# Optimization experiments

Measured on AMD Instinct MI355X. Metric: run time of the kernel, lower is better.

The kernel has to match this reference:

```python
import jax, jax.numpy as jnp
import numpy as np
from jax import lax


def _log_g(z):
    # log of g(x) = x + 0.5 if x >= 0 else sigmoid(x)
    return jnp.where(z >= 0, jnp.log(jax.nn.relu(z) + 0.5), -jax.nn.softplus(-z))


def setup_inputs() -> dict:
    key = jax.random.key(0)
    k1, k2, k3 = jax.random.split(key, 3)
    B, S, D, H = 8, 8192, 512, 256
    x = jax.random.normal(k1, (B, S, D), dtype=jnp.float32)
    h_prev = jax.random.normal(k2, (B, H), dtype=jnp.float32)
    # nn.Linear(D, 3H, bias=False) weight: [3H, D], scaled like torch default init
    W = jax.random.normal(k3, (3 * H, D), dtype=jnp.float32) * (1.0 / np.sqrt(D))
    return {"x": x, "h_prev": h_prev, "W": W}


def reference(x, h_prev, W):
    # x: [B,S,D], h_prev: [B,H], W: [3H,D]
    seq_len = x.shape[1]
    y = jnp.einsum("bsd,hd->bsh", x, W)              # [B,S,3H]
    f, i, h = jnp.split(y, 3, axis=-1)                # each [B,S,H]
    diff = jax.nn.softplus(-f) - jax.nn.softplus(-i)
    log_f = -jax.nn.softplus(diff)                    # log(sigmoid-normalized forget gate)
    log_i = -jax.nn.softplus(-diff)                   # log(input gate)
    log_h0 = _log_g(h_prev)                           # [B,H]
    log_tilde_h = _log_g(h)                           # [B,S,H]
    # parallel scan in log space: h_t = f_t * h_{t-1} + i_t * g(h_t~)
    a_star = jnp.concatenate(
        [jnp.zeros_like(log_h0)[:, None], jnp.cumsum(log_f, axis=1)], axis=1
    )                                                  # [B,S+1,H]
    log_vals = jnp.concatenate([log_h0[:, None], log_i + log_tilde_h], axis=1)  # [B,S+1,H]
    log_h = a_star + lax.cumlogsumexp(log_vals - a_star, axis=1)
    h_t = jnp.exp(log_h)                               # [B,S+1,H]
    return h_t[:, -seq_len:]                           # [B,S,H]
```

## Files before the change

### kernel.cpp

```cpp
#include <hip/hip_runtime.h>
#include <math.h>

#define BB 8
#define SS 8192
#define DD 512
#define HH 256
#define MM (BB * SS)
#define NN 768
#define CC 64
#define LL 128

typedef unsigned short u16;
typedef __attribute__((ext_vector_type(8))) short short8;
typedef __attribute__((ext_vector_type(4))) float f32x4;

#define AS1(p) ((const __attribute__((address_space(1))) void*)(p))
#define AS3(p) ((__attribute__((address_space(3))) void*)(p))

__device__ __forceinline__ u16 f2bf_rtne(float f) {
    union { float f; unsigned u; } v; v.f = f;
    unsigned r = v.u + 0x7fffu + ((v.u >> 16) & 1u);
    return (u16)(r >> 16);
}
__device__ __forceinline__ unsigned pack2_rtn(float a, float b) {
    union { float f; unsigned u; } x, y; x.f = a; y.f = b;
    return ((x.u + 0x8000u) >> 16) | ((y.u + 0x8000u) & 0xffff0000u);
}

__device__ __forceinline__ float sp_fast(float z) {
    return (z > 15.0f) ? z : __logf(1.0f + __expf(z));
}

__global__ __launch_bounds__(256) void convert_W(const float* __restrict__ W,
                                                 u16* __restrict__ Wr) {
    const int chunk = blockIdx.x * 256 + threadIdx.x;
    const int kh = chunk / 1536;
    const int rem = chunk % 1536;
    const int cl = rem >> 2, qq = rem & 3;
    const int kc = kh >> 1, half = kh & 1;
    const int c = half * 384 + cl;
    const int hg = c / 48, r48 = c % 48;
    const int g = r48 >> 4, hl = r48 & 15;
    const int wrow = g * HH + hg * 16 + hl;
    const int k0 = kc * 32 + qq * 8;
    const float4 v0 = *(const float4*)&W[(size_t)wrow * DD + k0];
    const float4 v1 = *(const float4*)&W[(size_t)wrow * DD + k0 + 4];
    u16 o[8];
    o[0]=f2bf_rtne(v0.x); o[1]=f2bf_rtne(v0.y); o[2]=f2bf_rtne(v0.z); o[3]=f2bf_rtne(v0.w);
    o[4]=f2bf_rtne(v1.x); o[5]=f2bf_rtne(v1.y); o[6]=f2bf_rtne(v1.z); o[7]=f2bf_rtne(v1.w);
    *(uint4*)&Wr[(size_t)chunk * 8] = *(const uint4*)o;
}

__global__ __launch_bounds__(512) void gemm_gate_mfma(
    const float* __restrict__ x,
    const u16* __restrict__ Wr,
    float* __restrict__ F_arr,
    float* __restrict__ u_out)
{
    __shared__ __align__(16) u16 Bs[2][12288];
    __shared__ __align__(16) u16 As[2][64 * 40];

    const int tid = threadIdx.x;
    const int m0 = blockIdx.x * 64;
    const int w = tid >> 6;
    const int lane = tid & 63;
    const int l16 = lane & 15;
    const int quad = lane >> 4;

    const int arow = tid >> 3;
    const int aqi = tid & 7;

    f32x4 acc[4][6];
    #pragma unroll
    for (int a = 0; a < 4; ++a)
        #pragma unroll
        for (int b = 0; b < 6; ++b)
            #pragma unroll
            for (int e = 0; e < 4; ++e) acc[a][b][e] = 0.0f;

    #pragma unroll
    for (int i = 0; i < 3; ++i) {
        const int idx = i * 512 + tid;
        __builtin_amdgcn_global_load_lds(AS1(Wr + (size_t)idx * 8),
                                         AS3(&Bs[0][idx * 8]), 16, 0, 0);
    }
    {
        const float4 v = *(const float4*)&x[(size_t)(m0 + arow) * DD + aqi * 4];
        *(uint2*)&As[0][arow * 40 + aqi * 4] =
            make_uint2(pack2_rtn(v.x, v.y), pack2_rtn(v.z, v.w));
    }
    float4 a_reg = *(const float4*)&x[(size_t)(m0 + arow) * DD + 32 + aqi * 4];
    __syncthreads();

    for (int kc = 0; kc < 16; ++kc) {
        {
            const size_t base = ((size_t)(kc * 2 + 1)) * 12288;
            #pragma unroll
            for (int i = 0; i < 3; ++i) {
                const int idx = i * 512 + tid;
                __builtin_amdgcn_global_load_lds(AS1(Wr + base + (size_t)idx * 8),
                                                 AS3(&Bs[1][idx * 8]), 16, 0, 0);
            }
        }
        short8 afr[4];
        #pragma unroll
        for (int mf = 0; mf < 4; ++mf)
            afr[mf] = *(const short8*)&As[kc & 1][(mf * 16 + l16) * 40 + quad * 8];

        {
            short8 bfr[3];
            #pragma unroll
            for (int jn = 0; jn < 3; ++jn)
                bfr[jn] = *(const short8*)&Bs[0][((w * 3 + jn) * 16 + l16) * 32 + quad * 8];
            #pragma unroll
            for (int mf = 0; mf < 4; ++mf)
                #pragma unroll
                for (int jn = 0; jn < 3; ++jn)
                    acc[mf][jn] = __builtin_amdgcn_mfma_f32_16x16x32_bf16(
                        afr[mf], bfr[jn], acc[mf][jn], 0, 0, 0);
        }
        *(uint2*)&As[(kc + 1) & 1][arow * 40 + aqi * 4] =
            make_uint2(pack2_rtn(a_reg.x, a_reg.y), pack2_rtn(a_reg.z, a_reg.w));
        {
            const int knext = (kc + 2 < 16) ? (kc + 2) : 15;
            a_reg = *(const float4*)&x[(size_t)(m0 + arow) * DD + knext * 32 + aqi * 4];
        }
        __syncthreads();

        if (kc < 15) {
            const size_t base = ((size_t)((kc + 1) * 2)) * 12288;
            #pragma unroll
            for (int i = 0; i < 3; ++i) {
                const int idx = i * 512 + tid;
                __builtin_amdgcn_global_load_lds(AS1(Wr + base + (size_t)idx * 8),
                                                 AS3(&Bs[0][idx * 8]), 16, 0, 0);
            }
        }
        {
            short8 bfr[3];
            #pragma unroll
            for (int jn = 0; jn < 3; ++jn)
                bfr[jn] = *(const short8*)&Bs[1][((w * 3 + jn) * 16 + l16) * 32 + quad * 8];
            #pragma unroll
            for (int mf = 0; mf < 4; ++mf)
                #pragma unroll
                for (int jn = 0; jn < 3; ++jn)
                    acc[mf][3 + jn] = __builtin_amdgcn_mfma_f32_16x16x32_bf16(
                        afr[mf], bfr[jn], acc[mf][3 + jn], 0, 0, 0);
        }
        __syncthreads();
    }

    #pragma unroll
    for (int half = 0; half < 2; ++half) {
        const int head = (half * 8 + w) * 16 + l16;
        #pragma unroll
        for (int mf = 0; mf < 4; ++mf) {
            #pragma unroll
            for (int r = 0; r < 4; ++r) {
                const int m = m0 + mf * 16 + quad * 4 + r;
                const float fr = acc[mf][half * 3 + 0][r];
                const float ir = acc[mf][half * 3 + 1][r];
                const float hr = acc[mf][half * 3 + 2][r];
                const float diff = sp_fast(-fr) - sp_fast(-ir);
                const float F = __builtin_amdgcn_rcpf(1.0f + __expf(diff));
                const float I = 1.0f - F;
                const float G = (hr >= 0.0f) ? (hr + 0.5f)
                                             : __builtin_amdgcn_rcpf(1.0f + __expf(-hr));
                const size_t o = (size_t)m * HH + head;
                F_arr[o] = F;
                u_out[o] = I * G;
            }
        }
    }
}

__global__ __launch_bounds__(256) void scan_pass1(
    const float* __restrict__ F_arr, const float* __restrict__ u_arr,
    float* __restrict__ P_arr, float* __restrict__ U_arr) {
    const int bc = blockIdx.x;
    const int b = bc / CC;
    const int c = bc % CC;
    const int h = threadIdx.x;
    size_t base = ((size_t)(b * SS + c * LL)) * HH + h;
    float P = 1.0f, U = 0.0f;
    #pragma unroll 4
    for (int t = 0; t < LL; ++t) {
        const float F = F_arr[base];
        const float u = u_arr[base];
        U = F * U + u;
        P = P * F;
        base += HH;
    }
    const size_t o = ((size_t)c * BB + b) * HH + h;
    P_arr[o] = P;
    U_arr[o] = U;
}

__global__ __launch_bounds__(256) void scan_pass2(
    const float* __restrict__ h_prev, const float* __restrict__ P_arr,
    const float* __restrict__ U_arr, float* __restrict__ Hin) {
    const int b = blockIdx.x;
    const int h = threadIdx.x;
    const float z = h_prev[b * HH + h];
    float carry = (z >= 0.0f) ? (z + 0.5f) : __builtin_amdgcn_rcpf(1.0f + __expf(-z));
    for (int c = 0; c < CC; ++c) {
        const size_t o = ((size_t)c * BB + b) * HH + h;
        Hin[o] = carry;
        carry = P_arr[o] * carry + U_arr[o];
    }
}

__global__ __launch_bounds__(256) void scan_pass3(
    const float* __restrict__ F_arr, const float* __restrict__ Hin,
    float* __restrict__ out) {
    const int bc = blockIdx.x;
    const int b = bc / CC;
    const int c = bc % CC;
    const int h = threadIdx.x;
    float hv = Hin[((size_t)c * BB + b) * HH + h];
    size_t base = ((size_t)(b * SS + c * LL)) * HH + h;
    #pragma unroll 4
    for (int t = 0; t < LL; ++t) {
        const float F = F_arr[base];
        const float u = out[base];
        hv = F * hv + u;
        out[base] = hv;
        base += HH;
    }
}

extern "C" void kernel_launch(void* const* d_in, const int* in_sizes, int n_in,
                              void* d_out, int out_size, void* d_ws, size_t ws_size,
                              hipStream_t stream) {
    const float* x      = (const float*)d_in[0];
    const float* h_prev = (const float*)d_in[1];
    const float* W      = (const float*)d_in[2];

    float* F_arr = (float*)d_ws;
    float* P_arr = F_arr + (size_t)MM * HH;
    float* U_arr = P_arr + (size_t)CC * BB * HH;
    float* Hin   = U_arr + (size_t)CC * BB * HH;
    u16*   Wr    = (u16*)(Hin + (size_t)CC * BB * HH);

    convert_W<<<192, 256, 0, stream>>>(W, Wr);
    gemm_gate_mfma<<<MM / 64, 512, 0, stream>>>(x, Wr, F_arr, (float*)d_out);
    scan_pass1<<<BB * CC, HH, 0, stream>>>(F_arr, (const float*)d_out, P_arr, U_arr);
    scan_pass2<<<BB, HH, 0, stream>>>(h_prev, P_arr, U_arr, Hin);
    scan_pass3<<<BB * CC, HH, 0, stream>>>(F_arr, Hin, (float*)d_out);
}
```

Baseline: 350.9 us.

## Triple-buffer GEMM W tiles with swizzled LDS and vectorize scan passes

The GEMM moves from double to triple buffering of the bf16 weight tiles in LDS. It uses explicit waitcnt/s_barrier pairs with sched barriers and raised MFMA priority, so global-to-LDS loads run further ahead of compute. The weight layout is XOR-swizzled in both convert_W and the fragment reads to reduce LDS bank conflicts. Separately, the scan passes now have each thread handle two adjacent hidden units with float2 loads and stores, using half as many blocks, and pass2 gets an unroll pragma. The hand-written vmcnt counts are fragile and a wrong count could let a tile be read before it has landed.

```diff
diff --git a/kernel.cpp b/kernel.cpp
--- a/kernel.cpp
+++ b/kernel.cpp
@@ -35,8 +35,9 @@
                                                  u16* __restrict__ Wr) {
     const int chunk = blockIdx.x * 256 + threadIdx.x;
     const int kh = chunk / 1536;
-    const int rem = chunk % 1536;
-    const int cl = rem >> 2, qq = rem & 3;
+    const int u = chunk % 1536;
+    const int cl = ((u >> 2) & ~1) | (((u >> 2) ^ (u >> 4)) & 1);
+    const int qq = (u & 3) ^ (cl & 3);
     const int kc = kh >> 1, half = kh & 1;
     const int c = half * 384 + cl;
     const int hg = c / 48, r48 = c % 48;
@@ -57,7 +58,7 @@
     float* __restrict__ F_arr,
     float* __restrict__ u_out)
 {
-    __shared__ __align__(16) u16 Bs[2][12288];
+    __shared__ __align__(16) u16 Bs[3][12288];
     __shared__ __align__(16) u16 As[2][64 * 40];
 
     const int tid = threadIdx.x;
@@ -78,77 +79,144 @@
             #pragma unroll
             for (int e = 0; e < 4; ++e) acc[a][b][e] = 0.0f;
 
+    int boff[3];
+    #pragma unroll
+    for (int jn = 0; jn < 3; ++jn) {
+        const int r = (w * 3 + jn) * 16 + l16;
+        boff[jn] = ((r * 4 + quad) ^ (r & 7)) * 8;
+    }
+
+    const float* xrow = &x[(size_t)(m0 + arow) * DD];
+
+    const float4 v0 = *(const float4*)&xrow[aqi * 4];
+    float4 a_reg = *(const float4*)&xrow[32 + aqi * 4];
+    asm volatile("" ::: "memory");
     #pragma unroll
     for (int i = 0; i < 3; ++i) {
         const int idx = i * 512 + tid;
         __builtin_amdgcn_global_load_lds(AS1(Wr + (size_t)idx * 8),
                                          AS3(&Bs[0][idx * 8]), 16, 0, 0);
     }
-    {
-        const float4 v = *(const float4*)&x[(size_t)(m0 + arow) * DD + aqi * 4];
-        *(uint2*)&As[0][arow * 40 + aqi * 4] =
-            make_uint2(pack2_rtn(v.x, v.y), pack2_rtn(v.z, v.w));
-    }
-    float4 a_reg = *(const float4*)&x[(size_t)(m0 + arow) * DD + 32 + aqi * 4];
-    __syncthreads();
-
-    for (int kc = 0; kc < 16; ++kc) {
-        {
-            const size_t base = ((size_t)(kc * 2 + 1)) * 12288;
-            #pragma unroll
-            for (int i = 0; i < 3; ++i) {
-                const int idx = i * 512 + tid;
-                __builtin_amdgcn_global_load_lds(AS1(Wr + base + (size_t)idx * 8),
-                                                 AS3(&Bs[1][idx * 8]), 16, 0, 0);
-            }
-        }
-        short8 afr[4];
+    #pragma unroll
+    for (int i = 0; i < 3; ++i) {
+        const int idx = i * 512 + tid;
+        __builtin_amdgcn_global_load_lds(AS1(Wr + 12288 + (size_t)idx * 8),
+                                         AS3(&Bs[1][idx * 8]), 16, 0, 0);
+    }
+    *(uint2*)&As[0][arow * 40 + aqi * 4] =
+        make_uint2(pack2_rtn(v0.x, v0.y), pack2_rtn(v0.z, v0.w));
+
+    int cur = 0;
+    short8 afr[4];
+    for (int kc = 0; kc < 15; ++kc) {
+        const int nb1 = (cur + 2 > 2) ? cur - 1 : cur + 2;
+        const int c1  = (cur + 1 > 2) ? 0 : cur + 1;
+
+        asm volatile("s_waitcnt lgkmcnt(0)" ::: "memory");
+        asm volatile("s_waitcnt vmcnt(3)" ::: "memory");
+        __builtin_amdgcn_s_barrier();
+        __builtin_amdgcn_sched_barrier(0);
         #pragma unroll
         for (int mf = 0; mf < 4; ++mf)
             afr[mf] = *(const short8*)&As[kc & 1][(mf * 16 + l16) * 40 + quad * 8];
-
-        {
-            short8 bfr[3];
-            #pragma unroll
-            for (int jn = 0; jn < 3; ++jn)
-                bfr[jn] = *(const short8*)&Bs[0][((w * 3 + jn) * 16 + l16) * 32 + quad * 8];
-            #pragma unroll
-            for (int mf = 0; mf < 4; ++mf)
-                #pragma unroll
-                for (int jn = 0; jn < 3; ++jn)
-                    acc[mf][jn] = __builtin_amdgcn_mfma_f32_16x16x32_bf16(
-                        afr[mf], bfr[jn], acc[mf][jn], 0, 0, 0);
-        }
+        short8 bfr[3];
+        #pragma unroll
+        for (int jn = 0; jn < 3; ++jn)
+            bfr[jn] = *(const short8*)&Bs[cur][boff[jn]];
         *(uint2*)&As[(kc + 1) & 1][arow * 40 + aqi * 4] =
             make_uint2(pack2_rtn(a_reg.x, a_reg.y), pack2_rtn(a_reg.z, a_reg.w));
         {
             const int knext = (kc + 2 < 16) ? (kc + 2) : 15;
-            a_reg = *(const float4*)&x[(size_t)(m0 + arow) * DD + knext * 32 + aqi * 4];
+            a_reg = *(const float4*)&xrow[knext * 32 + aqi * 4];
         }
-        __syncthreads();
-
-        if (kc < 15) {
-            const size_t base = ((size_t)((kc + 1) * 2)) * 12288;
+        {
+            const size_t gbase = (size_t)(2 * kc + 2) * 12288;
             #pragma unroll
             for (int i = 0; i < 3; ++i) {
                 const int idx = i * 512 + tid;
-                __builtin_amdgcn_global_load_lds(AS1(Wr + base + (size_t)idx * 8),
-                                                 AS3(&Bs[0][idx * 8]), 16, 0, 0);
+                __builtin_amdgcn_global_load_lds(AS1(Wr + gbase + (size_t)idx * 8),
+                                                 AS3(&Bs[nb1][idx * 8]), 16, 0, 0);
             }
         }
+        __builtin_amdgcn_sched_barrier(0);
+        __builtin_amdgcn_s_setprio(1);
+        #pragma unroll
+        for (int mf = 0; mf < 4; ++mf)
+            #pragma unroll
+            for (int jn = 0; jn < 3; ++jn)
+                acc[mf][jn] = __builtin_amdgcn_mfma_f32_16x16x32_bf16(
+                    afr[mf], bfr[jn], acc[mf][jn], 0, 0, 0);
+        __builtin_amdgcn_s_setprio(0);
+
+        asm volatile("s_waitcnt lgkmcnt(0)" ::: "memory");
+        asm volatile("s_waitcnt vmcnt(4)" ::: "memory");
+        __builtin_amdgcn_s_barrier();
+        __builtin_amdgcn_sched_barrier(0);
+        #pragma unroll
+        for (int jn = 0; jn < 3; ++jn)
+            bfr[jn] = *(const short8*)&Bs[c1][boff[jn]];
         {
-            short8 bfr[3];
+            const size_t gbase = (size_t)(2 * kc + 3) * 12288;
+            #pragma unroll
+            for (int i = 0; i < 3; ++i) {
+                const int idx = i * 512 + tid;
+                __builtin_amdgcn_global_load_lds(AS1(Wr + gbase + (size_t)idx * 8),
+                                                 AS3(&Bs[cur][idx * 8]), 16, 0, 0);
+            }
+        }
+        __builtin_amdgcn_sched_barrier(0);
+        __builtin_amdgcn_s_setprio(1);
+        #pragma unroll
+        for (int mf = 0; mf < 4; ++mf)
             #pragma unroll
             for (int jn = 0; jn < 3; ++jn)
-                bfr[jn] = *(const short8*)&Bs[1][((w * 3 + jn) * 16 + l16) * 32 + quad * 8];
-            #pragma unroll
-            for (int mf = 0; mf < 4; ++mf)
-                #pragma unroll
-                for (int jn = 0; jn < 3; ++jn)
-                    acc[mf][3 + jn] = __builtin_amdgcn_mfma_f32_16x16x32_bf16(
-                        afr[mf], bfr[jn], acc[mf][3 + jn], 0, 0, 0);
-        }
-        __syncthreads();
+                acc[mf][3 + jn] = __builtin_amdgcn_mfma_f32_16x16x32_bf16(
+                    afr[mf], bfr[jn], acc[mf][3 + jn], 0, 0, 0);
+        __builtin_amdgcn_s_setprio(0);
+
+        cur = nb1;
+    }
+    asm volatile("" :: "v"(a_reg.x), "v"(a_reg.y), "v"(a_reg.z), "v"(a_reg.w));
+
+    asm volatile("s_waitcnt lgkmcnt(0)" ::: "memory");
+    asm volatile("s_waitcnt vmcnt(3)" ::: "memory");
+    __builtin_amdgcn_s_barrier();
+    __builtin_amdgcn_sched_barrier(0);
+    #pragma unroll
+    for (int mf = 0; mf < 4; ++mf)
+        afr[mf] = *(const short8*)&As[1][(mf * 16 + l16) * 40 + quad * 8];
+    {
+        short8 bfr[3];
+        #pragma unroll
+        for (int jn = 0; jn < 3; ++jn)
+            bfr[jn] = *(const short8*)&Bs[cur][boff[jn]];
+        __builtin_amdgcn_s_setprio(1);
+        #pragma unroll
+        for (int mf = 0; mf < 4; ++mf)
+            #pragma unroll
+            for (int jn = 0; jn < 3; ++jn)
+                acc[mf][jn] = __builtin_amdgcn_mfma_f32_16x16x32_bf16(
+                    afr[mf], bfr[jn], acc[mf][jn], 0, 0, 0);
+        __builtin_amdgcn_s_setprio(0);
+    }
+    asm volatile("s_waitcnt lgkmcnt(0)" ::: "memory");
+    asm volatile("s_waitcnt vmcnt(0)" ::: "memory");
+    __builtin_amdgcn_s_barrier();
+    __builtin_amdgcn_sched_barrier(0);
+    {
+        const int c1 = (cur + 1 > 2) ? 0 : cur + 1;
+        short8 bfr[3];
+        #pragma unroll
+        for (int jn = 0; jn < 3; ++jn)
+            bfr[jn] = *(const short8*)&Bs[c1][boff[jn]];
+        __builtin_amdgcn_s_setprio(1);
+        #pragma unroll
+        for (int mf = 0; mf < 4; ++mf)
+            #pragma unroll
+            for (int jn = 0; jn < 3; ++jn)
+                acc[mf][3 + jn] = __builtin_amdgcn_mfma_f32_16x16x32_bf16(
+                    afr[mf], bfr[jn], acc[mf][3 + jn], 0, 0, 0);
+        __builtin_amdgcn_s_setprio(0);
     }
 
     #pragma unroll
@@ -178,23 +246,25 @@
 __global__ __launch_bounds__(256) void scan_pass1(
     const float* __restrict__ F_arr, const float* __restrict__ u_arr,
     float* __restrict__ P_arr, float* __restrict__ U_arr) {
-    const int bc = blockIdx.x;
-    const int b = bc / CC;
-    const int c = bc % CC;
-    const int h = threadIdx.x;
-    size_t base = ((size_t)(b * SS + c * LL)) * HH + h;
-    float P = 1.0f, U = 0.0f;
-    #pragma unroll 4
+    const int pair = blockIdx.x * 2 + (threadIdx.x >> 7);
+    const int b = pair / CC;
+    const int c = pair % CC;
+    const int h0 = (threadIdx.x & 127) * 2;
+    size_t base = ((size_t)(b * SS + c * LL)) * HH + h0;
+    float P0 = 1.0f, P1 = 1.0f, U0 = 0.0f, U1 = 0.0f;
+    #pragma unroll 8
     for (int t = 0; t < LL; ++t) {
-        const float F = F_arr[base];
-        const float u = u_arr[base];
-        U = F * U + u;
-        P = P * F;
+        const float2 F = *(const float2*)&F_arr[base];
+        const float2 u = *(const float2*)&u_arr[base];
+        U0 = F.x * U0 + u.x;
+        U1 = F.y * U1 + u.y;
+        P0 *= F.x;
+        P1 *= F.y;
         base += HH;
     }
-    const size_t o = ((size_t)c * BB + b) * HH + h;
-    P_arr[o] = P;
-    U_arr[o] = U;
+    const size_t o = ((size_t)c * BB + b) * HH + h0;
+    *(float2*)&P_arr[o] = make_float2(P0, P1);
+    *(float2*)&U_arr[o] = make_float2(U0, U1);
 }
 
 __global__ __launch_bounds__(256) void scan_pass2(
@@ -204,6 +274,7 @@
     const int h = threadIdx.x;
     const float z = h_prev[b * HH + h];
     float carry = (z >= 0.0f) ? (z + 0.5f) : __builtin_amdgcn_rcpf(1.0f + __expf(-z));
+    #pragma unroll 4
     for (int c = 0; c < CC; ++c) {
         const size_t o = ((size_t)c * BB + b) * HH + h;
         Hin[o] = carry;
@@ -214,18 +285,19 @@
 __global__ __launch_bounds__(256) void scan_pass3(
     const float* __restrict__ F_arr, const float* __restrict__ Hin,
     float* __restrict__ out) {
-    const int bc = blockIdx.x;
-    const int b = bc / CC;
-    const int c = bc % CC;
-    const int h = threadIdx.x;
-    float hv = Hin[((size_t)c * BB + b) * HH + h];
-    size_t base = ((size_t)(b * SS + c * LL)) * HH + h;
-    #pragma unroll 4
+    const int pair = blockIdx.x * 2 + (threadIdx.x >> 7);
+    const int b = pair / CC;
+    const int c = pair % CC;
+    const int h0 = (threadIdx.x & 127) * 2;
+    float2 hv = *(const float2*)&Hin[((size_t)c * BB + b) * HH + h0];
+    size_t base = ((size_t)(b * SS + c * LL)) * HH + h0;
+    #pragma unroll 8
     for (int t = 0; t < LL; ++t) {
-        const float F = F_arr[base];
-        const float u = out[base];
-        hv = F * hv + u;
-        out[base] = hv;
+        const float2 F = *(const float2*)&F_arr[base];
+        const float2 u = *(const float2*)&out[base];
+        hv.x = F.x * hv.x + u.x;
+        hv.y = F.y * hv.y + u.y;
+        *(float2*)&out[base] = hv;
         base += HH;
     }
 }
@@ -245,7 +317,7 @@
 
     convert_W<<<192, 256, 0, stream>>>(W, Wr);
     gemm_gate_mfma<<<MM / 64, 512, 0, stream>>>(x, Wr, F_arr, (float*)d_out);
-    scan_pass1<<<BB * CC, HH, 0, stream>>>(F_arr, (const float*)d_out, P_arr, U_arr);
+    scan_pass1<<<BB * CC / 2, 256, 0, stream>>>(F_arr, (const float*)d_out, P_arr, U_arr);
     scan_pass2<<<BB, HH, 0, stream>>>(h_prev, P_arr, U_arr, Hin);
-    scan_pass3<<<BB * CC, HH, 0, stream>>>(F_arr, Hin, (float*)d_out);
-}
+    scan_pass3<<<BB * CC / 2, 256, 0, stream>>>(F_arr, Hin, (float*)d_out);
+}
```

Measured after the change: 339.1 us. -3.4%, faster.

## Pack F/u as half2 in output buffer, split GEMM N across blocks, shorter scan chunks

Applied to the files above, without the earlier changes.

The gate GEMM now writes F and u as a packed fp16 pair into the output buffer instead of two fp32 arrays. This halves the intermediate traffic and drops the separate F workspace. The GEMM is split into four column blocks with 256 threads, an XOR-swizzled W layout, block-index remapping and s_setprio around the MFMAs. The scan uses 256 chunks of 32 steps and processes two heads per thread with vector loads. The fp16 storage of F and u lowers precision, which may hurt accuracy over long products, and the serial pass2 now runs four times more iterations.

```diff
diff --git a/kernel.cpp b/kernel.cpp
--- a/kernel.cpp
+++ b/kernel.cpp
@@ -1,4 +1,5 @@
 #include <hip/hip_runtime.h>
+#include <hip/hip_fp16.h>
 #include <math.h>
 
 #define BB 8
@@ -7,8 +8,8 @@
 #define HH 256
 #define MM (BB * SS)
 #define NN 768
-#define CC 64
-#define LL 128
+#define CC 256
+#define LL 32
 
 typedef unsigned short u16;
 typedef __attribute__((ext_vector_type(8))) short short8;
@@ -31,18 +32,30 @@
     return (z > 15.0f) ? z : __logf(1.0f + __expf(z));
 }
 
+__device__ __forceinline__ unsigned packFu(float F, float u) {
+    __half2 h = __floats2half2_rn(F, u);
+    return *reinterpret_cast<unsigned*>(&h);
+}
+__device__ __forceinline__ float2 unpackFu(unsigned v) {
+    __half2 h = *reinterpret_cast<__half2*>(&v);
+    return __half22float2(h);
+}
+
 __global__ __launch_bounds__(256) void convert_W(const float* __restrict__ W,
                                                  u16* __restrict__ Wr) {
     const int chunk = blockIdx.x * 256 + threadIdx.x;
-    const int kh = chunk / 1536;
-    const int rem = chunk % 1536;
-    const int cl = rem >> 2, qq = rem & 3;
-    const int kc = kh >> 1, half = kh & 1;
-    const int c = half * 384 + cl;
-    const int hg = c / 48, r48 = c % 48;
-    const int g = r48 >> 4, hl = r48 & 15;
-    const int wrow = g * HH + hg * 16 + hl;
-    const int k0 = kc * 32 + qq * 8;
+    const int kcb = chunk / 768;
+    const int u = chunk % 768;
+    const int kc = kcb >> 2, cb = kcb & 3;
+    const int v = u & 31;
+    const int s = ((v >> 2) & 7) ^ ((v >> 4) & 1);
+    const int q = (v & 3) ^ (s & 3);
+    const int r = ((u >> 5) << 3) | s;
+    const int w = r / 48;
+    const int rr = r % 48;
+    const int jn = rr >> 4, hl = rr & 15;
+    const int wrow = jn * HH + cb * 64 + w * 16 + hl;
+    const int k0 = kc * 32 + q * 8;
     const float4 v0 = *(const float4*)&W[(size_t)wrow * DD + k0];
     const float4 v1 = *(const float4*)&W[(size_t)wrow * DD + k0 + 4];
     u16 o[8];
@@ -51,150 +64,144 @@
     *(uint4*)&Wr[(size_t)chunk * 8] = *(const uint4*)o;
 }
 
-__global__ __launch_bounds__(512) void gemm_gate_mfma(
+__global__ __launch_bounds__(256, 4) void gemm_gate_mfma(
     const float* __restrict__ x,
     const u16* __restrict__ Wr,
-    float* __restrict__ F_arr,
-    float* __restrict__ u_out)
+    unsigned* __restrict__ Fu)
 {
-    __shared__ __align__(16) u16 Bs[2][12288];
+    __shared__ __align__(16) u16 Bs[2][6144];
     __shared__ __align__(16) u16 As[2][64 * 40];
 
     const int tid = threadIdx.x;
-    const int m0 = blockIdx.x * 64;
+    const int L = (blockIdx.x & 7) * 512 + (blockIdx.x >> 3);
+    const int mblk = L >> 2, cb = L & 3;
+    const int m0 = mblk * 64;
+
     const int w = tid >> 6;
     const int lane = tid & 63;
     const int l16 = lane & 15;
     const int quad = lane >> 4;
 
-    const int arow = tid >> 3;
-    const int aqi = tid & 7;
-
-    f32x4 acc[4][6];
+    const int arow = tid >> 2;
+    const int aqi = tid & 3;
+
+    f32x4 acc[4][3];
     #pragma unroll
     for (int a = 0; a < 4; ++a)
         #pragma unroll
-        for (int b = 0; b < 6; ++b)
+        for (int b = 0; b < 3; ++b)
             #pragma unroll
             for (int e = 0; e < 4; ++e) acc[a][b][e] = 0.0f;
 
+    int boff[3];
     #pragma unroll
-    for (int i = 0; i < 3; ++i) {
-        const int idx = i * 512 + tid;
-        __builtin_amdgcn_global_load_lds(AS1(Wr + (size_t)idx * 8),
-                                         AS3(&Bs[0][idx * 8]), 16, 0, 0);
-    }
+    for (int jn = 0; jn < 3; ++jn) {
+        const int r = w * 48 + jn * 16 + l16;
+        boff[jn] = (((r * 4 + quad) ^ (r & 7))) * 8;
+    }
+
+    const float* xrow = &x[(size_t)(m0 + arow) * DD];
+
     {
-        const float4 v = *(const float4*)&x[(size_t)(m0 + arow) * DD + aqi * 4];
-        *(uint2*)&As[0][arow * 40 + aqi * 4] =
-            make_uint2(pack2_rtn(v.x, v.y), pack2_rtn(v.z, v.w));
-    }
-    float4 a_reg = *(const float4*)&x[(size_t)(m0 + arow) * DD + 32 + aqi * 4];
+        const size_t ub = (size_t)(0 * 4 + cb) * 768;
+        #pragma unroll
+        for (int i = 0; i < 3; ++i) {
+            const int idx = i * 256 + tid;
+            __builtin_amdgcn_global_load_lds(AS1(Wr + (ub + idx) * 8),
+                                             AS3(&Bs[0][idx * 8]), 16, 0, 0);
+        }
+    }
+    float4 va0 = *(const float4*)&xrow[aqi * 8];
+    float4 va1 = *(const float4*)&xrow[aqi * 8 + 4];
+    float4 ar0 = *(const float4*)&xrow[32 + aqi * 8];
+    float4 ar1 = *(const float4*)&xrow[32 + aqi * 8 + 4];
+    {
+        uint4 p;
+        p.x = pack2_rtn(va0.x, va0.y); p.y = pack2_rtn(va0.z, va0.w);
+        p.z = pack2_rtn(va1.x, va1.y); p.w = pack2_rtn(va1.z, va1.w);
+        *(uint4*)&As[0][arow * 40 + aqi * 8] = p;
+    }
     __syncthreads();
 
     for (int kc = 0; kc < 16; ++kc) {
-        {
-            const size_t base = ((size_t)(kc * 2 + 1)) * 12288;
+        const int buf = kc & 1;
+        if (kc < 15) {
+            const size_t ub = (size_t)((kc + 1) * 4 + cb) * 768;
             #pragma unroll
             for (int i = 0; i < 3; ++i) {
-                const int idx = i * 512 + tid;
-                __builtin_amdgcn_global_load_lds(AS1(Wr + base + (size_t)idx * 8),
-                                                 AS3(&Bs[1][idx * 8]), 16, 0, 0);
+                const int idx = i * 256 + tid;
+                __builtin_amdgcn_global_load_lds(AS1(Wr + (ub + idx) * 8),
+                                                 AS3(&Bs[buf ^ 1][idx * 8]), 16, 0, 0);
+            }
+            uint4 p;
+            p.x = pack2_rtn(ar0.x, ar0.y); p.y = pack2_rtn(ar0.z, ar0.w);
+            p.z = pack2_rtn(ar1.x, ar1.y); p.w = pack2_rtn(ar1.z, ar1.w);
+            *(uint4*)&As[buf ^ 1][arow * 40 + aqi * 8] = p;
+            if (kc < 14) {
+                ar0 = *(const float4*)&xrow[(kc + 2) * 32 + aqi * 8];
+                ar1 = *(const float4*)&xrow[(kc + 2) * 32 + aqi * 8 + 4];
             }
         }
         short8 afr[4];
         #pragma unroll
         for (int mf = 0; mf < 4; ++mf)
-            afr[mf] = *(const short8*)&As[kc & 1][(mf * 16 + l16) * 40 + quad * 8];
-
-        {
-            short8 bfr[3];
+            afr[mf] = *(const short8*)&As[buf][(mf * 16 + l16) * 40 + quad * 8];
+        short8 bfr[3];
+        #pragma unroll
+        for (int jn = 0; jn < 3; ++jn)
+            bfr[jn] = *(const short8*)&Bs[buf][boff[jn]];
+
+        __builtin_amdgcn_s_setprio(1);
+        #pragma unroll
+        for (int mf = 0; mf < 4; ++mf)
             #pragma unroll
             for (int jn = 0; jn < 3; ++jn)
-                bfr[jn] = *(const short8*)&Bs[0][((w * 3 + jn) * 16 + l16) * 32 + quad * 8];
-            #pragma unroll
-            for (int mf = 0; mf < 4; ++mf)
-                #pragma unroll
-                for (int jn = 0; jn < 3; ++jn)
-                    acc[mf][jn] = __builtin_amdgcn_mfma_f32_16x16x32_bf16(
-                        afr[mf], bfr[jn], acc[mf][jn], 0, 0, 0);
+                acc[mf][jn] = __builtin_amdgcn_mfma_f32_16x16x32_bf16(
+                    afr[mf], bfr[jn], acc[mf][jn], 0, 0, 0);
+        __builtin_amdgcn_s_setprio(0);
+        __syncthreads();
+    }
+
+    const int head = cb * 64 + w * 16 + l16;
+    #pragma unroll
+    for (int mf = 0; mf < 4; ++mf) {
+        #pragma unroll
+        for (int r = 0; r < 4; ++r) {
+            const int m = m0 + mf * 16 + quad * 4 + r;
+            const float fr = acc[mf][0][r];
+            const float ir = acc[mf][1][r];
+            const float hr = acc[mf][2][r];
+            const float diff = sp_fast(-fr) - sp_fast(-ir);
+            const float F = __builtin_amdgcn_rcpf(1.0f + __expf(diff));
+            const float I = 1.0f - F;
+            const float G = (hr >= 0.0f) ? (hr + 0.5f)
+                                         : __builtin_amdgcn_rcpf(1.0f + __expf(-hr));
+            Fu[(size_t)m * HH + head] = packFu(F, I * G);
         }
-        *(uint2*)&As[(kc + 1) & 1][arow * 40 + aqi * 4] =
-            make_uint2(pack2_rtn(a_reg.x, a_reg.y), pack2_rtn(a_reg.z, a_reg.w));
-        {
-            const int knext = (kc + 2 < 16) ? (kc + 2) : 15;
-            a_reg = *(const float4*)&x[(size_t)(m0 + arow) * DD + knext * 32 + aqi * 4];
-        }
-        __syncthreads();
-
-        if (kc < 15) {
-            const size_t base = ((size_t)((kc + 1) * 2)) * 12288;
-            #pragma unroll
-            for (int i = 0; i < 3; ++i) {
-                const int idx = i * 512 + tid;
-                __builtin_amdgcn_global_load_lds(AS1(Wr + base + (size_t)idx * 8),
-                                                 AS3(&Bs[0][idx * 8]), 16, 0, 0);
-            }
-        }
-        {
-            short8 bfr[3];
-            #pragma unroll
-            for (int jn = 0; jn < 3; ++jn)
-                bfr[jn] = *(const short8*)&Bs[1][((w * 3 + jn) * 16 + l16) * 32 + quad * 8];
-            #pragma unroll
-            for (int mf = 0; mf < 4; ++mf)
-                #pragma unroll
-                for (int jn = 0; jn < 3; ++jn)
-                    acc[mf][3 + jn] = __builtin_amdgcn_mfma_f32_16x16x32_bf16(
-                        afr[mf], bfr[jn], acc[mf][3 + jn], 0, 0, 0);
-        }
-        __syncthreads();
-    }
-
-    #pragma unroll
-    for (int half = 0; half < 2; ++half) {
-        const int head = (half * 8 + w) * 16 + l16;
-        #pragma unroll
-        for (int mf = 0; mf < 4; ++mf) {
-            #pragma unroll
-            for (int r = 0; r < 4; ++r) {
-                const int m = m0 + mf * 16 + quad * 4 + r;
-                const float fr = acc[mf][half * 3 + 0][r];
-                const float ir = acc[mf][half * 3 + 1][r];
-                const float hr = acc[mf][half * 3 + 2][r];
-                const float diff = sp_fast(-fr) - sp_fast(-ir);
-                const float F = __builtin_amdgcn_rcpf(1.0f + __expf(diff));
-                const float I = 1.0f - F;
-                const float G = (hr >= 0.0f) ? (hr + 0.5f)
-                                             : __builtin_amdgcn_rcpf(1.0f + __expf(-hr));
-                const size_t o = (size_t)m * HH + head;
-                F_arr[o] = F;
-                u_out[o] = I * G;
-            }
-        }
     }
 }
 
 __global__ __launch_bounds__(256) void scan_pass1(
-    const float* __restrict__ F_arr, const float* __restrict__ u_arr,
+    const unsigned* __restrict__ Fu,
     float* __restrict__ P_arr, float* __restrict__ U_arr) {
-    const int bc = blockIdx.x;
-    const int b = bc / CC;
-    const int c = bc % CC;
-    const int h = threadIdx.x;
-    size_t base = ((size_t)(b * SS + c * LL)) * HH + h;
-    float P = 1.0f, U = 0.0f;
-    #pragma unroll 4
+    const int pair = blockIdx.x * 2 + (threadIdx.x >> 7);
+    const int b = pair / CC;
+    const int c = pair % CC;
+    const int h0 = (threadIdx.x & 127) * 2;
+    size_t base = ((size_t)(b * SS + c * LL)) * HH + h0;
+    float P0 = 1.0f, P1 = 1.0f, U0 = 0.0f, U1 = 0.0f;
+    #pragma unroll 8
     for (int t = 0; t < LL; ++t) {
-        const float F = F_arr[base];
-        const float u = u_arr[base];
-        U = F * U + u;
-        P = P * F;
+        const uint2 fu = *(const uint2*)&Fu[base];
+        const float2 a = unpackFu(fu.x);
+        const float2 d = unpackFu(fu.y);
+        U0 = a.x * U0 + a.y;  P0 *= a.x;
+        U1 = d.x * U1 + d.y;  P1 *= d.x;
         base += HH;
     }
-    const size_t o = ((size_t)c * BB + b) * HH + h;
-    P_arr[o] = P;
-    U_arr[o] = U;
+    const size_t o = ((size_t)c * BB + b) * HH + h0;
+    *(float2*)&P_arr[o] = make_float2(P0, P1);
+    *(float2*)&U_arr[o] = make_float2(U0, U1);
 }
 
 __global__ __launch_bounds__(256) void scan_pass2(
@@ -204,6 +211,7 @@
     const int h = threadIdx.x;
     const float z = h_prev[b * HH + h];
     float carry = (z >= 0.0f) ? (z + 0.5f) : __builtin_amdgcn_rcpf(1.0f + __expf(-z));
+    #pragma unroll 8
     for (int c = 0; c < CC; ++c) {
         const size_t o = ((size_t)c * BB + b) * HH + h;
         Hin[o] = carry;
@@ -212,20 +220,21 @@
 }
 
 __global__ __launch_bounds__(256) void scan_pass3(
-    const float* __restrict__ F_arr, const float* __restrict__ Hin,
-    float* __restrict__ out) {
-    const int bc = blockIdx.x;
-    const int b = bc / CC;
-    const int c = bc % CC;
-    const int h = threadIdx.x;
-    float hv = Hin[((size_t)c * BB + b) * HH + h];
-    size_t base = ((size_t)(b * SS + c * LL)) * HH + h;
-    #pragma unroll 4
+    const float* __restrict__ Hin, unsigned* buf) {
+    const int pair = blockIdx.x * 2 + (threadIdx.x >> 7);
+    const int b = pair / CC;
+    const int c = pair % CC;
+    const int h0 = (threadIdx.x & 127) * 2;
+    float2 hv = *(const float2*)&Hin[((size_t)c * BB + b) * HH + h0];
+    size_t base = ((size_t)(b * SS + c * LL)) * HH + h0;
+    #pragma unroll 8
     for (int t = 0; t < LL; ++t) {
-        const float F = F_arr[base];
-        const float u = out[base];
-        hv = F * hv + u;
-        out[base] = hv;
+        const uint2 fu = *(const uint2*)&buf[base];
+        const float2 a = unpackFu(fu.x);
+        const float2 d = unpackFu(fu.y);
+        hv.x = a.x * hv.x + a.y;
+        hv.y = d.x * hv.y + d.y;
+        *(float2*)&buf[base] = hv;
         base += HH;
     }
 }
@@ -237,15 +246,14 @@
     const float* h_prev = (const float*)d_in[1];
     const float* W      = (const float*)d_in[2];
 
-    float* F_arr = (float*)d_ws;
-    float* P_arr = F_arr + (size_t)MM * HH;
+    float* P_arr = (float*)d_ws;
     float* U_arr = P_arr + (size_t)CC * BB * HH;
     float* Hin   = U_arr + (size_t)CC * BB * HH;
     u16*   Wr    = (u16*)(Hin + (size_t)CC * BB * HH);
 
     convert_W<<<192, 256, 0, stream>>>(W, Wr);
-    gemm_gate_mfma<<<MM / 64, 512, 0, stream>>>(x, Wr, F_arr, (float*)d_out);
-    scan_pass1<<<BB * CC, HH, 0, stream>>>(F_arr, (const float*)d_out, P_arr, U_arr);
-    scan_pass2<<<BB, HH, 0, stream>>>(h_prev, P_arr, U_arr, Hin);
-    scan_pass3<<<BB * CC, HH, 0, stream>>>(F_arr, Hin, (float*)d_out);
-}
+    gemm_gate_mfma<<<4096, 256, 0, stream>>>(x, Wr, (unsigned*)d_out);
+    scan_pass1<<<BB * CC / 2, 256, 0, stream>>>((const unsigned*)d_out, P_arr, U_arr);
+    scan_pass2<<<BB, 256, 0, stream>>>(h_prev, P_arr, U_arr, Hin);
+    scan_pass3<<<BB * CC / 2, 256, 0, stream>>>(Hin, (unsigned*)d_out);
+}
```

After: 333.0 us. 1.05x faster.
